# Performance work log

Hardware: AMD Instinct MI355X
Metric: run time of the kernel (lower is better)

## Reference

```python
import jax, jax.numpy as jnp
import numpy as np

NUM_ENTITIES = 100000
NUM_TIMES = 10000
D = 512
DB = 768
NUM_REL = 200
NUM_BASES = 4
N_NODES = 30000
N_EDGES = 200000
B = 128
P_ENT = 64
P_TIME = 32
T_UNIQ = 2000


def setup_inputs() -> dict:
    key = jax.random.key(0)
    ks = jax.random.split(key, 32)
    n = jax.random.normal
    ri = jax.random.randint
    inp = {}
    # learned params
    inp['emb'] = n(ks[0], (NUM_ENTITIES + NUM_TIMES, D), jnp.float32) * 0.05
    sc = 1.0 / np.sqrt(D)
    inp['basis1'] = n(ks[1], (NUM_BASES, D, D), jnp.float32) * sc
    inp['att1'] = n(ks[2], (NUM_REL, NUM_BASES), jnp.float32) * 0.5
    inp['root1'] = n(ks[3], (D, D), jnp.float32) * sc
    inp['bias1'] = jnp.zeros((D,), jnp.float32)
    inp['basis2'] = n(ks[4], (NUM_BASES, D, D), jnp.float32) * sc
    inp['att2'] = n(ks[5], (NUM_REL, NUM_BASES), jnp.float32) * 0.5
    inp['root2'] = n(ks[6], (D, D), jnp.float32) * sc
    inp['bias2'] = jnp.zeros((D,), jnp.float32)
    sb = 1.0 / np.sqrt(DB)
    inp['W_lin'] = n(ks[7], (DB, D), jnp.float32) * sb
    inp['b_lin'] = jnp.zeros((D,), jnp.float32)
    inp['W_attn'] = n(ks[8], (DB, D), jnp.float32) * sb
    inp['b_attn'] = jnp.zeros((D,), jnp.float32)
    inp['W_prob'] = n(ks[9], (DB, 1), jnp.float32) * sb
    inp['b_prob'] = jnp.zeros((1,), jnp.float32)
    # forward tensor args
    inp['ques_emb_bert'] = n(ks[10], (B, DB), jnp.float32)
    inp['x_idx'] = ri(ks[11], (N_NODES,), 0, NUM_ENTITIES, jnp.int32)
    inp['edge_index'] = ri(ks[12], (2, N_EDGES), 0, N_NODES, jnp.int32)
    inp['edge_type'] = ri(ks[13], (N_EDGES,), 0, NUM_REL, jnp.int32)
    inp['start_time'] = ri(ks[14], (N_EDGES,), 0, NUM_TIMES, jnp.int32)
    inp['end_time'] = ri(ks[15], (N_EDGES,), 0, NUM_TIMES, jnp.int32)
    inp['edge_batch_idx'] = jnp.sort(ri(ks[16], (N_EDGES,), 0, B, jnp.int32))
    inp['edge_norm'] = jax.random.uniform(ks[17], (N_EDGES,), jnp.float32)
    inp['uniq_times'] = ri(ks[18], (T_UNIQ,), 0, NUM_TIMES, jnp.int32)
    # padded index vectors: positions >= count point at the appended zero row
    ent_counts = ri(ks[19], (B,), 1, P_ENT + 1, jnp.int32)
    time_counts = ri(ks[20], (B,), 1, P_TIME + 1, jnp.int32)
    pe = ri(ks[21], (B, P_ENT), 0, N_NODES, jnp.int32)
    pt = ri(ks[22], (B, P_TIME), 0, T_UNIQ, jnp.int32)
    inp['padded_ent'] = jnp.where(jnp.arange(P_ENT)[None, :] < ent_counts[:, None], pe, N_NODES)
    inp['padded_time'] = jnp.where(jnp.arange(P_TIME)[None, :] < time_counts[:, None], pt, T_UNIQ)
    inp['ent_counts'] = ent_counts
    inp['time_counts'] = time_counts
    return inp


def rgcn_layer(x, basis, att, root, bias, src, dst, etype, st_emb, et_emb, q_t, edge_norm):
    # basis decomposition: project all nodes through each basis once. [N, NB, D]
    xb = jnp.einsum('ni,bio->nbo', x, basis)
    coeff = att[etype]                                 # [E, NB]
    msg = jnp.einsum('eb,ebd->ed', coeff, xb[src])     # [E, D]
    # time gate: question-time embedding vs edge interval midpoint embedding
    gate = jax.nn.sigmoid(jnp.sum(q_t * 0.5 * (st_emb + et_emb), axis=-1))  # [E]
    msg = msg * (gate * edge_norm)[:, None]
    agg = jax.ops.segment_sum(msg, dst, num_segments=N_NODES)
    return agg + x @ root + bias


def reference(emb, basis1, att1, root1, bias1, basis2, att2, root2, bias2,
              W_lin, b_lin, W_attn, b_attn, W_prob, b_prob,
              ques_emb_bert, x_idx, edge_index, edge_type, start_time, end_time,
              edge_batch_idx, edge_norm, uniq_times, padded_ent, padded_time,
              ent_counts, time_counts):
    question_embedding = ques_emb_bert @ W_lin + b_lin                  # [B, D]
    time_for_edge_attn = (ques_emb_bert @ W_attn + b_attn)[edge_batch_idx]  # [E, D]
    st_emb = emb[start_time + NUM_ENTITIES]
    et_emb = emb[end_time + NUM_ENTITIES]
    x = emb[x_idx]                                                      # [N, D]
    src, dst = edge_index[0], edge_index[1]
    h = jax.nn.relu(rgcn_layer(x, basis1, att1, root1, bias1, src, dst, edge_type,
                               st_emb, et_emb, time_for_edge_attn, edge_norm))
    # dropout is identity in eval mode
    h = rgcn_layer(h, basis2, att2, root2, bias2, src, dst, edge_type,
                   st_emb, et_emb, time_for_edge_attn, edge_norm)       # [N, D]
    subgraph_time_emb = emb[uniq_times + NUM_ENTITIES]                  # [T_u, D]
    zero = jnp.zeros((1, D), h.dtype)
    ent_w_zeros = jnp.concatenate([h, zero], axis=0)
    time_w_zeros = jnp.concatenate([subgraph_time_emb, zero], axis=0)
    pooled_ent = jnp.sum(ent_w_zeros[padded_ent], axis=1) / ent_counts[:, None].astype(h.dtype)
    pooled_time = jnp.sum(time_w_zeros[padded_time], axis=1) / time_counts[:, None].astype(h.dtype)
    p_ent = jax.nn.sigmoid(ques_emb_bert @ W_prob + b_prob)             # [B, 1]
    pred = (question_embedding + pooled_ent * p_ent + pooled_time * (1.0 - p_ent)) / 3.0
    # batched cosine similarity against full entity+time vocab
    pred_n = pred / jnp.maximum(jnp.linalg.norm(pred, axis=-1, keepdims=True), 1e-8)
    emb_n = emb / jnp.maximum(jnp.linalg.norm(emb, axis=-1, keepdims=True), 1e-8)
    score = pred_n @ emb_n.T                                            # [B, V]
    return score * 30.0
```

## Files before the change

### kernel.cpp

```cpp
#include <hip/hip_runtime.h>

#define NUM_ENT   100000
#define NTIMES    10000
#define DD        512
#define DB        768
#define NREL      200
#define NBAS      4
#define NN        30000
#define NEDGE     200000
#define BATCH     128
#define PENT      64
#define PTIME     32
#define TUNIQ     2000
#define V_TOT     110000
#define M_PAD2    30208
#define MT2R      1888
#define KT_L      80
#define KT_E      16
#define TCT       632

typedef __attribute__((ext_vector_type(8))) short s8v;
typedef __attribute__((ext_vector_type(4))) float f4v;

__device__ __forceinline__ unsigned short f2bf(float x){
  unsigned int u = __builtin_bit_cast(unsigned int, x);
  u += 0x7fffu + ((u >> 16) & 1u);
  return (unsigned short)(u >> 16);
}
__device__ __forceinline__ float bf2f(unsigned short h){
  unsigned int u = ((unsigned int)h) << 16;
  return __builtin_bit_cast(float, u);
}

__device__ __forceinline__ void gload16(const void* g, void* l){
  __builtin_amdgcn_global_load_lds(
      (const __attribute__((address_space(1))) void*)g,
      (__attribute__((address_space(3))) void*)l, 16, 0, 0);
}


__global__ __launch_bounds__(256) void k_small2(const float* __restrict__ ques,
    const float* __restrict__ Wl, const float* __restrict__ bl,
    const float* __restrict__ Wa, const float* __restrict__ ba,
    const float* __restrict__ Wp, const float* __restrict__ bp,
    float* __restrict__ qlin, float* __restrict__ qattn, float* __restrict__ pent){
  if (blockIdx.x == 32){
    int b = threadIdx.x >> 1, half = threadIdx.x & 1;
    float a = 0.f;
    int k0 = half * 384;
    for (int k = k0; k < k0 + 384; ++k)
      a = fmaf(ques[(size_t)b * DB + k], Wp[k], a);
    a += __shfl_xor(a, 1);
    if (half == 0) pent[b] = 1.f / (1.f + expf(-(a + bp[0])));
    return;
  }
  __shared__ float sq[128 * 96];
  int col = threadIdx.x & 31, bg = threadIdx.x >> 5;
  int c0 = blockIdx.x * 32;
  const float* W = (c0 < 512) ? Wl : Wa;
  int wcol = (c0 & 511) + col;
  float acc[16] = {};
  for (int k0 = 0; k0 < DB; k0 += 96){
    __syncthreads();
    for (int i = threadIdx.x; i < 128 * 96; i += 256){
      int b = i / 96, kk = i - b * 96;
      sq[i] = ques[(size_t)b * DB + k0 + kk];
    }
    __syncthreads();
    for (int kk = 0; kk < 96; kk += 4){
      float w0 = W[(size_t)(k0 + kk + 0) * 512 + wcol];
      float w1 = W[(size_t)(k0 + kk + 1) * 512 + wcol];
      float w2 = W[(size_t)(k0 + kk + 2) * 512 + wcol];
      float w3 = W[(size_t)(k0 + kk + 3) * 512 + wcol];
      #pragma unroll
      for (int bb = 0; bb < 16; ++bb){
        float4 qv = *reinterpret_cast<const float4*>(&sq[(bg * 16 + bb) * 96 + kk]);
        acc[bb] = fmaf(qv.x, w0, fmaf(qv.y, w1, fmaf(qv.z, w2, fmaf(qv.w, w3, acc[bb]))));
      }
    }
  }
  float* dst = (c0 < 512) ? qlin : qattn;
  const float* bias = (c0 < 512) ? bl : ba;
  #pragma unroll
  for (int bb = 0; bb < 16; ++bb)
    dst[(size_t)(bg * 16 + bb) * 512 + wcol] = acc[bb] + bias[wcol];
}

__global__ __launch_bounds__(256) void k_pack_qrows(const float* __restrict__ src,
    unsigned short* __restrict__ Ap){
  int w = (int)((blockIdx.x * 256 + threadIdx.x) >> 6);
  int lane = threadIdx.x & 63;
  if (w >= BATCH) return;
  const float* p = src + (size_t)w * 512 + lane * 8;
  s8v o;
  #pragma unroll
  for (int j = 0; j < 8; ++j) o[j] = (short)f2bf(p[j]);
  *reinterpret_cast<s8v*>(Ap + ((size_t)((w >> 4) * KT_E + (lane >> 2)) << 9)
                             + ((w & 15) + (lane & 3) * 16) * 8) = o;
}

__global__ __launch_bounds__(256) void k_pack_B(const float* __restrict__ basis,
    const float* __restrict__ root, unsigned short* __restrict__ Bp){
  int idx = blockIdx.x * 256 + threadIdx.x;
  if (idx >= KT_L * 32 * 64) return;
  int lane = idx & 63; int kt = idx >> 11;
  int k0 = kt * 32 + (lane >> 4) * 8;
  int col = ((idx >> 6) & 31) * 16 + (lane & 15);
  s8v o;
  #pragma unroll
  for (int j = 0; j < 8; ++j){
    int k = k0 + j;
    float v = (k < 2048) ? basis[(size_t)k * 512 + col] : root[(size_t)(k - 2048) * 512 + col];
    o[j] = (short)f2bf(v);
  }
  *reinterpret_cast<s8v*>(Bp + (size_t)idx * 8) = o;
}

__global__ __launch_bounds__(256) void k_pack_temb(const float* __restrict__ emb,
    unsigned short* __restrict__ Bt){
  int idx = blockIdx.x * 256 + threadIdx.x;
  if (idx >= KT_E * TCT * 64) return;
  int lane = idx & 63;
  int ct = (idx >> 6) % TCT;
  int kt = idx / (TCT * 64);
  int c = ct * 16 + (lane & 15);
  int k0 = kt * 32 + (lane >> 4) * 8;
  s8v o;
  if (c < NTIMES){
    const float* p = emb + (size_t)(NUM_ENT + c) * 512 + k0;
    #pragma unroll
    for (int j = 0; j < 8; ++j) o[j] = (short)f2bf(p[j]);
  } else {
    #pragma unroll
    for (int j = 0; j < 8; ++j) o[j] = 0;
  }
  *reinterpret_cast<s8v*>(Bt + (size_t)idx * 8) = o;
}

__global__ __launch_bounds__(256) void k_gemm_m2(
    const unsigned short* __restrict__ A, const unsigned short* __restrict__ B,
    float* __restrict__ outf){
  __shared__ __align__(1024) short sAll[3 * 8192];
  const int Kt = KT_E;
  int tid = threadIdx.x;
  int lane = tid & 63, wid = tid >> 6;
  int wr = wid >> 1, wc = wid & 1;
  int rt0 = blockIdx.x * 8;
  int ct0 = blockIdx.y * 8;
  const unsigned short* pA0 = A + ((size_t)(rt0 + 2 * wid) * Kt) * 512 + lane * 8;
  const unsigned short* pA1 = pA0 + (size_t)Kt * 512;
  const unsigned short* pB0 = B + (size_t)(ct0 + 2 * wid) * 512 + lane * 8;
  const unsigned short* pB1 = pB0 + 512;
  size_t gbs = (size_t)TCT * 512;
  int so = 2 * wid * 512;
  f4v acc[4][4] = {};

  auto STAGE = [&](int buf, int kt){
    short* b = &sAll[buf * 8192];
    gload16(pA0 + (size_t)kt * 512, b + so);
    gload16(pA1 + (size_t)kt * 512, b + so + 512);
    gload16(pB0 + (size_t)kt * gbs, b + 4096 + so);
    gload16(pB1 + (size_t)kt * gbs, b + 4096 + so + 512);
  };
  auto COMPUTE = [&](int buf){
    const short* base = &sAll[buf * 8192];
    s8v af[4], bfr[4];
    #pragma unroll
    for (int m = 0; m < 4; ++m) af[m] = *reinterpret_cast<const s8v*>(base + (wr * 4 + m) * 512 + lane * 8);
    #pragma unroll
    for (int n = 0; n < 4; ++n) bfr[n] = *reinterpret_cast<const s8v*>(base + 4096 + (wc * 4 + n) * 512 + lane * 8);
    #pragma unroll
    for (int m = 0; m < 4; ++m)
      #pragma unroll
      for (int n = 0; n < 4; ++n)
        acc[m][n] = __builtin_amdgcn_mfma_f32_16x16x32_bf16(af[m], bfr[n], acc[m][n], 0, 0, 0);
  };

  STAGE(0, 0);
  STAGE(1, 1);
  int cb = 0, sb = 2;
  for (int kt = 0; kt < Kt - 2; ++kt){
    STAGE(sb, kt + 2);
    asm volatile("s_waitcnt vmcnt(8)" ::: "memory");
    __builtin_amdgcn_s_barrier();
    __builtin_amdgcn_sched_barrier(0);
    COMPUTE(cb);
    __builtin_amdgcn_s_barrier();
    cb = (cb == 2) ? 0 : cb + 1;
    sb = (sb == 2) ? 0 : sb + 1;
  }
  asm volatile("s_waitcnt vmcnt(4)" ::: "memory");
  __builtin_amdgcn_s_barrier();
  __builtin_amdgcn_sched_barrier(0);
  COMPUTE(cb);
  cb = (cb == 2) ? 0 : cb + 1;
  asm volatile("s_waitcnt vmcnt(0)" ::: "memory");
  __builtin_amdgcn_s_barrier();
  __builtin_amdgcn_sched_barrier(0);
  COMPUTE(cb);

  #pragma unroll
  for (int m = 0; m < 4; ++m)
    #pragma unroll
    for (int n = 0; n < 4; ++n){
      int row0 = rt0 * 16 + (wr * 4 + m) * 16 + ((lane >> 4) * 4);
      int col  = (ct0 + wc * 4 + n) * 16 + (lane & 15);
      #pragma unroll
      for (int r = 0; r < 4; ++r){
        int rr = row0 + r;
        if (col < NTIMES) outf[(size_t)rr * NTIMES + col] = acc[m][n][r];
      }
    }
}

template<int MODE>
__global__ __launch_bounds__(512, 4) void k_gemm256(
    const unsigned short* __restrict__ A, const unsigned short* __restrict__ B,
    const float* __restrict__ bias, unsigned short* __restrict__ outh){
  __shared__ __align__(1024) short sAll[3 * 12288];
  const int Kt = KT_L;
  int tid = threadIdx.x;
  int lane = tid & 63, wid = tid >> 6;
  int wr = wid >> 1, wc = wid & 1;
  int g = blockIdx.x;
  int ng = (g & 7) * 59 + (g >> 3);
  int blkM = ng >> 2, blkN = ng & 3;
  int rt0 = blkM * 16;
  int ct0 = blkN * 8;
  const unsigned short* pA0 = A + ((size_t)(rt0 + wid) * Kt) * 512 + lane * 8;
  const unsigned short* pA1 = A + ((size_t)(rt0 + 8 + wid) * Kt) * 512 + lane * 8;
  const unsigned short* pB0 = B + (size_t)(ct0 + wid) * 512 + lane * 8;
  const size_t gbs = 32 * 512;
  int soA0 = wid * 512, soA1 = (8 + wid) * 512, soB = 8192 + wid * 512;
  f4v acc[4][4] = {};

  auto STAGE = [&](int buf, int kt){
    short* b = &sAll[buf * 12288];
    gload16(pA0 + (size_t)kt * 512, b + soA0);
    gload16(pA1 + (size_t)kt * 512, b + soA1);
    gload16(pB0 + (size_t)kt * gbs, b + soB);
  };
  auto COMPUTE = [&](int buf){
    const short* base = &sAll[buf * 12288];
    s8v af[4], bfr[4];
    #pragma unroll
    for (int m = 0; m < 4; ++m) af[m] = *reinterpret_cast<const s8v*>(base + (wr * 4 + m) * 512 + lane * 8);
    #pragma unroll
    for (int n = 0; n < 4; ++n) bfr[n] = *reinterpret_cast<const s8v*>(base + 8192 + (wc * 4 + n) * 512 + lane * 8);
    __builtin_amdgcn_s_setprio(1);
    #pragma unroll
    for (int m = 0; m < 4; ++m)
      #pragma unroll
      for (int n = 0; n < 4; ++n)
        acc[m][n] = __builtin_amdgcn_mfma_f32_16x16x32_bf16(af[m], bfr[n], acc[m][n], 0, 0, 0);
    __builtin_amdgcn_s_setprio(0);
  };

  STAGE(0, 0);
  STAGE(1, 1);
  int cb = 0, sb = 2;
  for (int kt = 0; kt < Kt - 2; ++kt){
    STAGE(sb, kt + 2);
    asm volatile("s_waitcnt vmcnt(6)" ::: "memory");
    __builtin_amdgcn_s_barrier();
    __builtin_amdgcn_sched_barrier(0);
    COMPUTE(cb);
    __builtin_amdgcn_s_barrier();
    cb = (cb == 2) ? 0 : cb + 1;
    sb = (sb == 2) ? 0 : sb + 1;
  }
  asm volatile("s_waitcnt vmcnt(3)" ::: "memory");
  __builtin_amdgcn_s_barrier();
  __builtin_amdgcn_sched_barrier(0);
  COMPUTE(cb);
  cb = (cb == 2) ? 0 : cb + 1;
  asm volatile("s_waitcnt vmcnt(0)" ::: "memory");
  __builtin_amdgcn_s_barrier();
  __builtin_amdgcn_sched_barrier(0);
  COMPUTE(cb);

  int R0 = blkM * 256 + wr * 64 + (lane >> 4) * 4;
  int C0 = blkN * 128 + wc * 64 + (lane & 15);
  #pragma unroll
  for (int m = 0; m < 4; ++m)
    #pragma unroll
    for (int r4 = 0; r4 < 4; ++r4){
      int rr = R0 + m * 16 + r4;
      if (rr < NN){
        #pragma unroll
        for (int n = 0; n < 4; ++n){
          int col = C0 + n * 16;
          float v = acc[m][n][r4] + bias[col];
          if constexpr (MODE == 1) v = fmaxf(v, 0.f);
          outh[(size_t)rr * 512 + col] = f2bf(v);
        }
// ... 77 lines not shown
    s8v xv = *reinterpret_cast<const s8v*>(xsrc + (size_t)s0 * 512 + lane * 8);
    for (int j = 0; j < deg; ++j){
      s8v xn = xv;
      if (j + 1 < deg){
        int sn = __shfl(my_s, j + 1);
        xn = *reinterpret_cast<const s8v*>(xsrc + (size_t)sn * 512 + lane * 8);
      }
      float c0 = __shfl(c0l, j), c1 = __shfl(c1l, j);
      float c2 = __shfl(c2l, j), c3 = __shfl(c3l, j);
      #pragma unroll
      for (int jj = 0; jj < 8; ++jj){
        float x = bf2f((unsigned short)xv[jj]);
        acc[0][jj] = fmaf(c0, x, acc[0][jj]);
        acc[1][jj] = fmaf(c1, x, acc[1][jj]);
        acc[2][jj] = fmaf(c2, x, acc[2][jj]);
        acc[3][jj] = fmaf(c3, x, acc[3][jj]);
      }
      xv = xn;
    }
  }
  #pragma unroll
  for (int b = 0; b < NBAS; ++b){
    s8v o;
    #pragma unroll
    for (int jj = 0; jj < 8; ++jj) o[jj] = (short)f2bf(acc[b][jj]);
    *reinterpret_cast<s8v*>(Ap + ((size_t)(n >> 4) * KT_L + b * 16 + (lane >> 2)) * 512
                               + ((n & 15) + (lane & 3) * 16) * 8) = o;
  }
}

__global__ __launch_bounds__(256) void k_pred(const unsigned short* __restrict__ h2,
    const float* __restrict__ emb, const int* __restrict__ uniq,
    const int* __restrict__ pent_idx, const int* __restrict__ ptime_idx,
    const int* __restrict__ ent_c, const int* __restrict__ time_c,
    const float* __restrict__ qlin, const float* __restrict__ pent,
    unsigned short* __restrict__ Ap_pred){
  __shared__ float sacc[4][512];
  int b = blockIdx.x;
  int wid = threadIdx.x >> 6, lane = threadIdx.x & 63;
  float a[8] = {};
  if (wid < 2){
    for (int j = wid * 32; j < wid * 32 + 32; ++j){
      int idx = pent_idx[b * PENT + j];
      if (idx < NN){
        s8v hv = *reinterpret_cast<const s8v*>(h2 + (size_t)idx * 512 + lane * 8);
        #pragma unroll
        for (int jj = 0; jj < 8; ++jj) a[jj] += bf2f((unsigned short)hv[jj]);
      }
    }
  } else {
    for (int j = (wid - 2) * 16; j < (wid - 2) * 16 + 16; ++j){
      int ti = ptime_idx[b * PTIME + j];
      if (ti < TUNIQ){
        const float* p = emb + (size_t)(NUM_ENT + uniq[ti]) * 512 + lane * 8;
        #pragma unroll
        for (int jj = 0; jj < 8; ++jj) a[jj] += p[jj];
      }
    }
  }
  #pragma unroll
  for (int jj = 0; jj < 8; ++jj) sacc[wid][lane * 8 + jj] = a[jj];
  __syncthreads();
  if (wid == 0){
    float ce = 1.f / (float)ent_c[b], ct = 1.f / (float)time_c[b];
    float p = pent[b];
    float pr[8]; float ss = 0.f;
    #pragma unroll
    for (int jj = 0; jj < 8; ++jj){
      int i = lane * 8 + jj;
      float ae = sacc[0][i] + sacc[1][i];
      float at = sacc[2][i] + sacc[3][i];
      float v = (qlin[(size_t)b * 512 + i] + ae * ce * p + at * ct * (1.f - p)) * (1.f / 3.f);
      pr[jj] = v; ss += v * v;
    }
    ss += __shfl_xor(ss, 32); ss += __shfl_xor(ss, 16); ss += __shfl_xor(ss, 8);
    ss += __shfl_xor(ss, 4);  ss += __shfl_xor(ss, 2);  ss += __shfl_xor(ss, 1);
    float inv = 1.f / fmaxf(sqrtf(ss), 1e-8f);
    s8v o;
    #pragma unroll
    for (int jj = 0; jj < 8; ++jj) o[jj] = (short)f2bf(pr[jj] * inv);
    *reinterpret_cast<s8v*>(Ap_pred + ((size_t)((b >> 4) * KT_E + (lane >> 2)) << 9)
                                    + ((b & 15) + (lane & 3) * 16) * 8) = o;
  }
}

__global__ __launch_bounds__(256, 3) void k_score(
    const unsigned short* __restrict__ Apred, const float* __restrict__ emb,
    float* __restrict__ out){
  __shared__ __align__(1024) short sB[2][4096];
  __shared__ float sf[256];
  int tid = threadIdx.x;
  int lane = tid & 63, wid = tid >> 6;
  int wr = wid >> 1, wc = wid & 1;
  int c0 = blockIdx.x * 128;
  int bc = tid & 127;
  int kh = tid >> 7;
  int colg = c0 + bc;
  bool cval = colg < V_TOT;
  const float* gB = emb + (size_t)colg * 512 + kh * 16;
  int wb0 = (bc >> 4) * 512 + ((2 * kh) * 16 + (bc & 15)) * 8;
  int wb1 = wb0 + 128;
  float ss = 0.f;
  float4 q0, q1, q2, q3;
  f4v acc[4][4] = {};

  auto LOADB = [&](int s){
    if (cval){
      const float4* p = reinterpret_cast<const float4*>(gB + (size_t)s * 32);
      q0 = p[0]; q1 = p[1]; q2 = p[2]; q3 = p[3];
    } else {
      q0 = q1 = q2 = q3 = float4{0.f, 0.f, 0.f, 0.f};
    }
  };
  auto WRITEB = [&](int p){
    short* bb = &sB[p][0];
    s8v o0, o1;
    o0[0] = (short)f2bf(q0.x); o0[1] = (short)f2bf(q0.y); o0[2] = (short)f2bf(q0.z); o0[3] = (short)f2bf(q0.w);
    o0[4] = (short)f2bf(q1.x); o0[5] = (short)f2bf(q1.y); o0[6] = (short)f2bf(q1.z); o0[7] = (short)f2bf(q1.w);
    o1[0] = (short)f2bf(q2.x); o1[1] = (short)f2bf(q2.y); o1[2] = (short)f2bf(q2.z); o1[3] = (short)f2bf(q2.w);
    o1[4] = (short)f2bf(q3.x); o1[5] = (short)f2bf(q3.y); o1[6] = (short)f2bf(q3.z); o1[7] = (short)f2bf(q3.w);
    ss += q0.x*q0.x + q0.y*q0.y + q0.z*q0.z + q0.w*q0.w;
    ss += q1.x*q1.x + q1.y*q1.y + q1.z*q1.z + q1.w*q1.w;
    ss += q2.x*q2.x + q2.y*q2.y + q2.z*q2.z + q2.w*q2.w;
    ss += q3.x*q3.x + q3.y*q3.y + q3.z*q3.z + q3.w*q3.w;
    *reinterpret_cast<s8v*>(bb + wb0) = o0;
    *reinterpret_cast<s8v*>(bb + wb1) = o1;
  };
  auto COMPUTE = [&](int p, int s){
    s8v af[4], bfr[4];
    #pragma unroll
    for (int m = 0; m < 4; ++m)
      af[m] = *reinterpret_cast<const s8v*>(
          Apred + (((size_t)(wr * 4 + m) * KT_E + s) << 9) + lane * 8);
    #pragma unroll
    for (int n = 0; n < 4; ++n)
      bfr[n] = *reinterpret_cast<const s8v*>(&sB[p][(wc * 4 + n) * 512 + lane * 8]);
    #pragma unroll
    for (int m = 0; m < 4; ++m)
      #pragma unroll
      for (int n = 0; n < 4; ++n)
        acc[m][n] = __builtin_amdgcn_mfma_f32_16x16x32_bf16(af[m], bfr[n], acc[m][n], 0, 0, 0);
  };

  LOADB(0);
  for (int s = 0; s < 16; ++s){
    int p = s & 1;
    WRITEB(p);
    __syncthreads();
    if (s < 15) LOADB(s + 1);
    COMPUTE(p, s);
    __syncthreads();
  }
  sf[tid] = ss;
  __syncthreads();

  int R0 = wr * 64 + (lane >> 4) * 4;
  int C0l = wc * 64 + (lane & 15);
  float inv[4];
  #pragma unroll
  for (int n = 0; n < 4; ++n){
    int cl = C0l + n * 16;
    float s2 = sf[cl] + sf[cl + 128];
    inv[n] = (1.f / fmaxf(sqrtf(s2), 1e-8f)) * 30.0f;
  }
  bool cok = (c0 + 127) < V_TOT;
  #pragma unroll
  for (int m = 0; m < 4; ++m)
    #pragma unroll
    for (int r4 = 0; r4 < 4; ++r4){
      int rr = R0 + m * 16 + r4;
      float* orow = out + (size_t)rr * V_TOT + c0 + C0l;
      if (cok){
        #pragma unroll
        for (int n = 0; n < 4; ++n) orow[n * 16] = acc[m][n][r4] * inv[n];
      } else {
        #pragma unroll
        for (int n = 0; n < 4; ++n)
          if (c0 + C0l + n * 16 < V_TOT) orow[n * 16] = acc[m][n][r4] * inv[n];
      }
    }
}

extern "C" void kernel_launch(void* const* d_in, const int* in_sizes, int n_in,
                              void* d_out, int out_size, void* d_ws, size_t ws_size,
                              hipStream_t stream){
  const float* emb    = (const float*)d_in[0];
  const float* basis1 = (const float*)d_in[1];
  const float* att1   = (const float*)d_in[2];
  const float* root1  = (const float*)d_in[3];
  const float* bias1  = (const float*)d_in[4];
  const float* basis2 = (const float*)d_in[5];
  const float* att2   = (const float*)d_in[6];
  const float* root2  = (const float*)d_in[7];
  const float* bias2  = (const float*)d_in[8];
  const float* W_lin  = (const float*)d_in[9];
  const float* b_lin  = (const float*)d_in[10];
  const float* W_attn = (const float*)d_in[11];
  const float* b_attn = (const float*)d_in[12];
  const float* W_prob = (const float*)d_in[13];
  const float* b_prob = (const float*)d_in[14];
  const float* ques   = (const float*)d_in[15];
  const int* x_idx    = (const int*)d_in[16];
  const int* eidx     = (const int*)d_in[17];
  const int* etype    = (const int*)d_in[18];
  const int* stime    = (const int*)d_in[19];
  const int* etime    = (const int*)d_in[20];
  const int* ebatch   = (const int*)d_in[21];
  const float* enorm  = (const float*)d_in[22];
  const int* uniq     = (const int*)d_in[23];
  const int* pent_i   = (const int*)d_in[24];
  const int* ptime_i  = (const int*)d_in[25];
  const int* ent_c    = (const int*)d_in[26];
  const int* time_c   = (const int*)d_in[27];
  float* out = (float*)d_out;

  char* w = (char*)d_ws;
  size_t off = 0;
  auto alloc = [&](size_t bytes)->char*{ char* p = w + off; off += (bytes + 255) & ~(size_t)255; return p; };
  unsigned short* Ap   = (unsigned short*)alloc((size_t)MT2R * KT_L * 1024);
  unsigned short* B1p  = (unsigned short*)alloc((size_t)KT_L * 32 * 1024);
  unsigned short* B2p  = (unsigned short*)alloc((size_t)KT_L * 32 * 1024);
  unsigned short* Bt   = (unsigned short*)alloc((size_t)KT_E * TCT * 1024);
  char* xh_base = alloc((size_t)NN * 512 * 2 * 2);
  unsigned short* x_rm = (unsigned short*)xh_base;
  unsigned short* h1   = (unsigned short*)(xh_base + (size_t)NN * 512 * 2);
  unsigned short* h2   = (unsigned short*)xh_base;
  float* M2    = (float*)alloc((size_t)BATCH * NTIMES * 4);
  float* we    = (float*)alloc((size_t)NEDGE * 4);
  float* qlin  = (float*)alloc((size_t)BATCH * 512 * 4);
  float* qattn = (float*)alloc((size_t)BATCH * 512 * 4);
  float* pent  = (float*)alloc(1024);
  unsigned short* Apq    = (unsigned short*)alloc((size_t)8 * KT_E * 1024);
  unsigned short* Appred = (unsigned short*)alloc((size_t)8 * KT_E * 1024);
  int* cnt   = (int*)alloc((size_t)NN * 4);
  int* lists = (int*)alloc((size_t)NN * 64 * 4);
  (void)ws_size; (void)in_sizes; (void)n_in; (void)out_size;

  k_small2<<<33, 256, 0, stream>>>(ques, W_lin, b_lin, W_attn, b_attn, W_prob, b_prob,
                                   qlin, qattn, pent);
  k_pack_qrows<<<32, 256, 0, stream>>>(qattn, Apq);
  k_pack_B<<<(KT_L * 32 * 64 + 255) / 256, 256, 0, stream>>>(basis1, root1, B1p);
  k_pack_B<<<(KT_L * 32 * 64 + 255) / 256, 256, 0, stream>>>(basis2, root2, B2p);
  k_pack_temb<<<(KT_E * TCT * 64) / 256, 256, 0, stream>>>(emb, Bt);
  k_gemm_m2<<<dim3(1, 79), 256, 0, stream>>>(Apq, Bt, M2);
  hipMemsetAsync(cnt, 0, (size_t)NN * 4, stream);
  k_edgeprep<<<(NEDGE + 255) / 256, 256, 0, stream>>>(ebatch, stime, etime, enorm, M2,
                                                      eidx, we, cnt, lists);
  k_gather_x<<<NN / 4, 256, 0, stream>>>(x_idx, emb, Ap, x_rm);
  k_edge_agg<<<NN / 4, 256, 0, stream>>>(x_rm, eidx, etype, we, att1, cnt, lists, Ap);
  k_gemm256<1><<<472, 512, 0, stream>>>(Ap, B1p, bias1, h1);
  k_pack_rows<<<NN / 4, 256, 0, stream>>>(h1, Ap);
  k_edge_agg<<<NN / 4, 256, 0, stream>>>(h1, eidx, etype, we, att2, cnt, lists, Ap);
  k_gemm256<2><<<472, 512, 0, stream>>>(Ap, B2p, bias2, h2);
  k_pred<<<BATCH, 256, 0, stream>>>(h2, emb, uniq, pent_i, ptime_i, ent_c, time_c,
                                    qlin, pent, Appred);
  k_score<<<860, 256, 0, stream>>>(Appred, emb, out);
}
```

Baseline: 713.3 us.

## Replace packed time-embedding GEMM and score GEMM with LDS-free column-per-wave GEMM

Adds a templated k_colgemm in which each wavefront owns 32 vocabulary columns. It streams fp32 embedding rows straight from global memory into registers, converts them to bf16 and feeds MFMA, while the A fragments (128 query rows) are read directly from global memory. This one kernel replaces both the time-embedding pack plus M2 GEMM and the final cosine-score kernel, which removes a pack pass, a workspace buffer and LDS staging and barriers. In exchange, A fragments are re-read from global/L2 by every wave, and the store pattern writes scattered 4-byte values per row.

```diff
diff --git a/kernel.cpp b/kernel.cpp
--- a/kernel.cpp
+++ b/kernel.cpp
@@ -17,7 +17,6 @@
 #define MT2R      1888
 #define KT_L      80
 #define KT_E      16
-#define TCT       632
 
 typedef __attribute__((ext_vector_type(8))) short s8v;
 typedef __attribute__((ext_vector_type(4))) float f4v;
@@ -116,100 +115,86 @@
   *reinterpret_cast<s8v*>(Bp + (size_t)idx * 8) = o;
 }
 
-__global__ __launch_bounds__(256) void k_pack_temb(const float* __restrict__ emb,
-    unsigned short* __restrict__ Bt){
-  int idx = blockIdx.x * 256 + threadIdx.x;
-  if (idx >= KT_E * TCT * 64) return;
-  int lane = idx & 63;
-  int ct = (idx >> 6) % TCT;
-  int kt = idx / (TCT * 64);
-  int c = ct * 16 + (lane & 15);
-  int k0 = kt * 32 + (lane >> 4) * 8;
-  s8v o;
-  if (c < NTIMES){
-    const float* p = emb + (size_t)(NUM_ENT + c) * 512 + k0;
-    #pragma unroll
-    for (int j = 0; j < 8; ++j) o[j] = (short)f2bf(p[j]);
-  } else {
-    #pragma unroll
-    for (int j = 0; j < 8; ++j) o[j] = 0;
-  }
-  *reinterpret_cast<s8v*>(Bt + (size_t)idx * 8) = o;
-}
-
-__global__ __launch_bounds__(256) void k_gemm_m2(
-    const unsigned short* __restrict__ A, const unsigned short* __restrict__ B,
-    float* __restrict__ outf){
-  __shared__ __align__(1024) short sAll[3 * 8192];
-  const int Kt = KT_E;
-  int tid = threadIdx.x;
-  int lane = tid & 63, wid = tid >> 6;
-  int wr = wid >> 1, wc = wid & 1;
-  int rt0 = blockIdx.x * 8;
-  int ct0 = blockIdx.y * 8;
-  const unsigned short* pA0 = A + ((size_t)(rt0 + 2 * wid) * Kt) * 512 + lane * 8;
-  const unsigned short* pA1 = pA0 + (size_t)Kt * 512;
-  const unsigned short* pB0 = B + (size_t)(ct0 + 2 * wid) * 512 + lane * 8;
-  const unsigned short* pB1 = pB0 + 512;
-  size_t gbs = (size_t)TCT * 512;
-  int so = 2 * wid * 512;
-  f4v acc[4][4] = {};
-
-  auto STAGE = [&](int buf, int kt){
-    short* b = &sAll[buf * 8192];
-    gload16(pA0 + (size_t)kt * 512, b + so);
-    gload16(pA1 + (size_t)kt * 512, b + so + 512);
-    gload16(pB0 + (size_t)kt * gbs, b + 4096 + so);
-    gload16(pB1 + (size_t)kt * gbs, b + 4096 + so + 512);
-  };
-  auto COMPUTE = [&](int buf){
-    const short* base = &sAll[buf * 8192];
-    s8v af[4], bfr[4];
-    #pragma unroll
-    for (int m = 0; m < 4; ++m) af[m] = *reinterpret_cast<const s8v*>(base + (wr * 4 + m) * 512 + lane * 8);
-    #pragma unroll
-    for (int n = 0; n < 4; ++n) bfr[n] = *reinterpret_cast<const s8v*>(base + 4096 + (wc * 4 + n) * 512 + lane * 8);
-    #pragma unroll
-    for (int m = 0; m < 4; ++m)
-      #pragma unroll
-      for (int n = 0; n < 4; ++n)
-        acc[m][n] = __builtin_amdgcn_mfma_f32_16x16x32_bf16(af[m], bfr[n], acc[m][n], 0, 0, 0);
-  };
-
-  STAGE(0, 0);
-  STAGE(1, 1);
-  int cb = 0, sb = 2;
-  for (int kt = 0; kt < Kt - 2; ++kt){
-    STAGE(sb, kt + 2);
-    asm volatile("s_waitcnt vmcnt(8)" ::: "memory");
-    __builtin_amdgcn_s_barrier();
-    __builtin_amdgcn_sched_barrier(0);
-    COMPUTE(cb);
-    __builtin_amdgcn_s_barrier();
-    cb = (cb == 2) ? 0 : cb + 1;
-    sb = (sb == 2) ? 0 : sb + 1;
-  }
-  asm volatile("s_waitcnt vmcnt(4)" ::: "memory");
-  __builtin_amdgcn_s_barrier();
-  __builtin_amdgcn_sched_barrier(0);
-  COMPUTE(cb);
-  cb = (cb == 2) ? 0 : cb + 1;
-  asm volatile("s_waitcnt vmcnt(0)" ::: "memory");
-  __builtin_amdgcn_s_barrier();
-  __builtin_amdgcn_sched_barrier(0);
-  COMPUTE(cb);
-
-  #pragma unroll
-  for (int m = 0; m < 4; ++m)
-    #pragma unroll
-    for (int n = 0; n < 4; ++n){
-      int row0 = rt0 * 16 + (wr * 4 + m) * 16 + ((lane >> 4) * 4);
-      int col  = (ct0 + wc * 4 + n) * 16 + (lane & 15);
-      #pragma unroll
-      for (int r = 0; r < 4; ++r){
-        int rr = row0 + r;
-        if (col < NTIMES) outf[(size_t)rr * NTIMES + col] = acc[m][n][r];
-      }
+template<int NORM>
+__global__ __launch_bounds__(256, 4) void k_colgemm(
+    const unsigned short* __restrict__ Ap, const float* __restrict__ embbase,
+    float* __restrict__ out, int ncols, int ldout){
+  int lane = threadIdx.x & 63, wid = threadIdx.x >> 6;
+  int w32 = (blockIdx.x * 4 + wid) * 32;
+  if (w32 >= ncols) return;
+  int r16 = lane & 15, kq = lane >> 4;
+  int c0 = w32 + r16, c1 = w32 + 16 + r16;
+  bool rv0 = c0 < ncols, rv1 = c1 < ncols;
+  const float* gB0 = embbase + (size_t)c0 * 512 + kq * 8;
+  const float* gB1 = embbase + (size_t)c1 * 512 + kq * 8;
+  f4v acc0[8], acc1[8];
+  #pragma unroll
+  for (int m = 0; m < 8; ++m){ acc0[m] = f4v{0,0,0,0}; acc1[m] = f4v{0,0,0,0}; }
+  float ss0 = 0.f, ss1 = 0.f;
+  float cu0[8], cu1[8], nx0[8], nx1[8];
+
+  #pragma unroll
+  for (int j = 0; j < 4; ++j){
+    float4 a0 = rv0 ? reinterpret_cast<const float4*>(gB0)[j & 1 ? 1 : 0]
+                    : float4{0,0,0,0};
+    (void)a0;
+  }
+  {
+    float4 a0 = rv0 ? reinterpret_cast<const float4*>(gB0)[0] : float4{0,0,0,0};
+    float4 a1 = rv0 ? reinterpret_cast<const float4*>(gB0)[1] : float4{0,0,0,0};
+    float4 b0 = rv1 ? reinterpret_cast<const float4*>(gB1)[0] : float4{0,0,0,0};
+    float4 b1 = rv1 ? reinterpret_cast<const float4*>(gB1)[1] : float4{0,0,0,0};
+    cu0[0]=a0.x; cu0[1]=a0.y; cu0[2]=a0.z; cu0[3]=a0.w;
+    cu0[4]=a1.x; cu0[5]=a1.y; cu0[6]=a1.z; cu0[7]=a1.w;
+    cu1[0]=b0.x; cu1[1]=b0.y; cu1[2]=b0.z; cu1[3]=b0.w;
+    cu1[4]=b1.x; cu1[5]=b1.y; cu1[6]=b1.z; cu1[7]=b1.w;
+  }
+  #pragma unroll
+  for (int kt = 0; kt < 16; ++kt){
+    if (kt < 15){
+      const float4* p0 = reinterpret_cast<const float4*>(gB0 + (kt + 1) * 32);
+      const float4* p1 = reinterpret_cast<const float4*>(gB1 + (kt + 1) * 32);
+      float4 a0 = rv0 ? p0[0] : float4{0,0,0,0};
+      float4 a1 = rv0 ? p0[1] : float4{0,0,0,0};
+      float4 b0 = rv1 ? p1[0] : float4{0,0,0,0};
+      float4 b1 = rv1 ? p1[1] : float4{0,0,0,0};
+      nx0[0]=a0.x; nx0[1]=a0.y; nx0[2]=a0.z; nx0[3]=a0.w;
+      nx0[4]=a1.x; nx0[5]=a1.y; nx0[6]=a1.z; nx0[7]=a1.w;
+      nx1[0]=b0.x; nx1[1]=b0.y; nx1[2]=b0.z; nx1[3]=b0.w;
+      nx1[4]=b1.x; nx1[5]=b1.y; nx1[6]=b1.z; nx1[7]=b1.w;
+    }
+    s8v bf0, bf1;
+    #pragma unroll
+    for (int j = 0; j < 8; ++j){
+      ss0 = fmaf(cu0[j], cu0[j], ss0);
+      ss1 = fmaf(cu1[j], cu1[j], ss1);
+      bf0[j] = (short)f2bf(cu0[j]);
+      bf1[j] = (short)f2bf(cu1[j]);
+    }
+    #pragma unroll
+    for (int m = 0; m < 8; ++m){
+      s8v af = *reinterpret_cast<const s8v*>(Ap + ((size_t)(m * KT_E + kt) << 9) + lane * 8);
+      acc0[m] = __builtin_amdgcn_mfma_f32_16x16x32_bf16(af, bf0, acc0[m], 0, 0, 0);
+      acc1[m] = __builtin_amdgcn_mfma_f32_16x16x32_bf16(af, bf1, acc1[m], 0, 0, 0);
+    }
+    #pragma unroll
+    for (int j = 0; j < 8; ++j){ cu0[j] = nx0[j]; cu1[j] = nx1[j]; }
+  }
+  float inv0 = 1.f, inv1 = 1.f;
+  if constexpr (NORM){
+    ss0 += __shfl_xor(ss0, 16); ss0 += __shfl_xor(ss0, 32);
+    ss1 += __shfl_xor(ss1, 16); ss1 += __shfl_xor(ss1, 32);
+    inv0 = 30.f / fmaxf(sqrtf(ss0), 1e-8f);
+    inv1 = 30.f / fmaxf(sqrtf(ss1), 1e-8f);
+  }
+  #pragma unroll
+  for (int m = 0; m < 8; ++m)
+    #pragma unroll
+    for (int r = 0; r < 4; ++r){
+      int row = m * 16 + kq * 4 + r;
+      float* orow = out + (size_t)row * ldout;
+      if (rv0) orow[c0] = acc0[m][r] * inv0;
+      if (rv1) orow[c1] = acc1[m][r] * inv1;
     }
 }
 
@@ -456,103 +441,6 @@
   }
 }
 
-__global__ __launch_bounds__(256, 3) void k_score(
-    const unsigned short* __restrict__ Apred, const float* __restrict__ emb,
-    float* __restrict__ out){
-  __shared__ __align__(1024) short sB[2][4096];
-  __shared__ float sf[256];
-  int tid = threadIdx.x;
-  int lane = tid & 63, wid = tid >> 6;
-  int wr = wid >> 1, wc = wid & 1;
-  int c0 = blockIdx.x * 128;
-  int bc = tid & 127;
-  int kh = tid >> 7;
-  int colg = c0 + bc;
-  bool cval = colg < V_TOT;
-  const float* gB = emb + (size_t)colg * 512 + kh * 16;
-  int wb0 = (bc >> 4) * 512 + ((2 * kh) * 16 + (bc & 15)) * 8;
-  int wb1 = wb0 + 128;
-  float ss = 0.f;
-  float4 q0, q1, q2, q3;
-  f4v acc[4][4] = {};
-
-  auto LOADB = [&](int s){
-    if (cval){
-      const float4* p = reinterpret_cast<const float4*>(gB + (size_t)s * 32);
-      q0 = p[0]; q1 = p[1]; q2 = p[2]; q3 = p[3];
-    } else {
-      q0 = q1 = q2 = q3 = float4{0.f, 0.f, 0.f, 0.f};
-    }
-  };
-  auto WRITEB = [&](int p){
-    short* bb = &sB[p][0];
-    s8v o0, o1;
-    o0[0] = (short)f2bf(q0.x); o0[1] = (short)f2bf(q0.y); o0[2] = (short)f2bf(q0.z); o0[3] = (short)f2bf(q0.w);
-    o0[4] = (short)f2bf(q1.x); o0[5] = (short)f2bf(q1.y); o0[6] = (short)f2bf(q1.z); o0[7] = (short)f2bf(q1.w);
-    o1[0] = (short)f2bf(q2.x); o1[1] = (short)f2bf(q2.y); o1[2] = (short)f2bf(q2.z); o1[3] = (short)f2bf(q2.w);
-    o1[4] = (short)f2bf(q3.x); o1[5] = (short)f2bf(q3.y); o1[6] = (short)f2bf(q3.z); o1[7] = (short)f2bf(q3.w);
-    ss += q0.x*q0.x + q0.y*q0.y + q0.z*q0.z + q0.w*q0.w;
-    ss += q1.x*q1.x + q1.y*q1.y + q1.z*q1.z + q1.w*q1.w;
-    ss += q2.x*q2.x + q2.y*q2.y + q2.z*q2.z + q2.w*q2.w;
-    ss += q3.x*q3.x + q3.y*q3.y + q3.z*q3.z + q3.w*q3.w;
-    *reinterpret_cast<s8v*>(bb + wb0) = o0;
-    *reinterpret_cast<s8v*>(bb + wb1) = o1;
-  };
-  auto COMPUTE = [&](int p, int s){
-    s8v af[4], bfr[4];
-    #pragma unroll
-    for (int m = 0; m < 4; ++m)
-      af[m] = *reinterpret_cast<const s8v*>(
-          Apred + (((size_t)(wr * 4 + m) * KT_E + s) << 9) + lane * 8);
-    #pragma unroll
-    for (int n = 0; n < 4; ++n)
-      bfr[n] = *reinterpret_cast<const s8v*>(&sB[p][(wc * 4 + n) * 512 + lane * 8]);
-    #pragma unroll
-    for (int m = 0; m < 4; ++m)
-      #pragma unroll
-      for (int n = 0; n < 4; ++n)
-        acc[m][n] = __builtin_amdgcn_mfma_f32_16x16x32_bf16(af[m], bfr[n], acc[m][n], 0, 0, 0);
-  };
-
-  LOADB(0);
-  for (int s = 0; s < 16; ++s){
-    int p = s & 1;
-    WRITEB(p);
-    __syncthreads();
-    if (s < 15) LOADB(s + 1);
-    COMPUTE(p, s);
-    __syncthreads();
-  }
-  sf[tid] = ss;
-  __syncthreads();
-
-  int R0 = wr * 64 + (lane >> 4) * 4;
-  int C0l = wc * 64 + (lane & 15);
-  float inv[4];
-  #pragma unroll
-  for (int n = 0; n < 4; ++n){
-    int cl = C0l + n * 16;
-    float s2 = sf[cl] + sf[cl + 128];
-    inv[n] = (1.f / fmaxf(sqrtf(s2), 1e-8f)) * 30.0f;
-  }
-  bool cok = (c0 + 127) < V_TOT;
-  #pragma unroll
-  for (int m = 0; m < 4; ++m)
-    #pragma unroll
-    for (int r4 = 0; r4 < 4; ++r4){
-      int rr = R0 + m * 16 + r4;
-      float* orow = out + (size_t)rr * V_TOT + c0 + C0l;
-      if (cok){
-        #pragma unroll
-        for (int n = 0; n < 4; ++n) orow[n * 16] = acc[m][n][r4] * inv[n];
-      } else {
-        #pragma unroll
-        for (int n = 0; n < 4; ++n)
-          if (c0 + C0l + n * 16 < V_TOT) orow[n * 16] = acc[m][n][r4] * inv[n];
-      }
-    }
-}
-
 extern "C" void kernel_launch(void* const* d_in, const int* in_sizes, int n_in,
                               void* d_out, int out_size, void* d_ws, size_t ws_size,
                               hipStream_t stream){
@@ -592,7 +480,6 @@
   unsigned short* Ap   = (unsigned short*)alloc((size_t)MT2R * KT_L * 1024);
   unsigned short* B1p  = (unsigned short*)alloc((size_t)KT_L * 32 * 1024);
   unsigned short* B2p  = (unsigned short*)alloc((size_t)KT_L * 32 * 1024);
-  unsigned short* Bt   = (unsigned short*)alloc((size_t)KT_E * TCT * 1024);
   char* xh_base = alloc((size_t)NN * 512 * 2 * 2);
   unsigned short* x_rm = (unsigned short*)xh_base;
   unsigned short* h1   = (unsigned short*)(xh_base + (size_t)NN * 512 * 2);
@@ -613,8 +500,8 @@
   k_pack_qrows<<<32, 256, 0, stream>>>(qattn, Apq);
   k_pack_B<<<(KT_L * 32 * 64 + 255) / 256, 256, 0, stream>>>(basis1, root1, B1p);
   k_pack_B<<<(KT_L * 32 * 64 + 255) / 256, 256, 0, stream>>>(basis2, root2, B2p);
-  k_pack_temb<<<(KT_E * TCT * 64) / 256, 256, 0, stream>>>(emb, Bt);
-  k_gemm_m2<<<dim3(1, 79), 256, 0, stream>>>(Apq, Bt, M2);
+  k_colgemm<0><<<(10000 / 32 + 4) / 4, 256, 0, stream>>>(
+      Apq, emb + (size_t)NUM_ENT * 512, M2, NTIMES, NTIMES);
   hipMemsetAsync(cnt, 0, (size_t)NN * 4, stream);
   k_edgeprep<<<(NEDGE + 255) / 256, 256, 0, stream>>>(ebatch, stime, etime, enorm, M2,
                                                       eidx, we, cnt, lists);
@@ -626,5 +513,6 @@
   k_gemm256<2><<<472, 512, 0, stream>>>(Ap, B2p, bias2, h2);
   k_pred<<<BATCH, 256, 0, stream>>>(h2, emb, uniq, pent_i, ptime_i, ent_c, time_c,
                                     qlin, pent, Appred);
-  k_score<<<860, 256, 0, stream>>>(Appred, emb, out);
-}
+  k_colgemm<1><<<(V_TOT / 32 + 4) / 4, 256, 0, stream>>>(
+      Appred, emb, out, V_TOT, V_TOT);
+}
```

New measurement: 895.3 us. +25.5%, slower.

## Pre-pack full embedding table to bf16 tiles and share with time GEMM and scoring

Applied to the files above, without the earlier changes.

Adds a conversion kernel that converts the full entity+time embedding table to bf16 in MFMA tile layout once and computes per-row inverse norms. The time-embedding GEMM now reads its slice of that packed table, which removes the separate time-embedding pack. The final scoring kernel is replaced by a pipelined async global-to-LDS GEMM that stages both operands through LDS and writes coalesced float4 output through an LDS transpose. This costs an extra round trip of the bf16 table through memory (about 110MB written and read back) in exchange for a simpler, better pipelined scoring loop.

```diff
diff --git a/kernel.cpp b/kernel.cpp
--- a/kernel.cpp
+++ b/kernel.cpp
@@ -13,11 +13,12 @@
 #define PTIME     32
 #define TUNIQ     2000
 #define V_TOT     110000
+#define V_PAD     110208
+#define VT16      6888
 #define M_PAD2    30208
 #define MT2R      1888
 #define KT_L      80
 #define KT_E      16
-#define TCT       632
 
 typedef __attribute__((ext_vector_type(8))) short s8v;
 typedef __attribute__((ext_vector_type(4))) float f4v;
@@ -38,6 +39,43 @@
       (__attribute__((address_space(3))) void*)l, 16, 0, 0);
 }
 
+
+__global__ __launch_bounds__(256) void k_conv_emb(const float* __restrict__ emb,
+    unsigned short* __restrict__ Bp, float* __restrict__ invn){
+  int vt = blockIdx.x;
+  int wid = threadIdx.x >> 6, lane = threadIdx.x & 63;
+  int vrow = vt * 16 + (lane & 15);
+  float ss = 0.f;
+  __shared__ float ssw[4][16];
+  for (int i = 0; i < 4; ++i){
+    int kt = wid + i * 4;
+    int k0 = kt * 32 + (lane >> 4) * 8;
+    s8v o;
+    if (vrow < V_TOT){
+      const float4* p = reinterpret_cast<const float4*>(emb + (size_t)vrow * DD + k0);
+      float4 v0 = p[0], v1 = p[1];
+      ss += v0.x*v0.x + v0.y*v0.y + v0.z*v0.z + v0.w*v0.w;
+      ss += v1.x*v1.x + v1.y*v1.y + v1.z*v1.z + v1.w*v1.w;
+      o[0] = (short)f2bf(v0.x); o[1] = (short)f2bf(v0.y);
+      o[2] = (short)f2bf(v0.z); o[3] = (short)f2bf(v0.w);
+      o[4] = (short)f2bf(v1.x); o[5] = (short)f2bf(v1.y);
+      o[6] = (short)f2bf(v1.z); o[7] = (short)f2bf(v1.w);
+    } else {
+      #pragma unroll
+      for (int j = 0; j < 8; ++j) o[j] = 0;
+    }
+    *reinterpret_cast<s8v*>(Bp + ((size_t)(kt * VT16 + vt) << 9) + lane * 8) = o;
+  }
+  ss += __shfl_xor(ss, 16);
+  ss += __shfl_xor(ss, 32);
+  if ((lane >> 4) == 0) ssw[wid][lane] = ss;
+  __syncthreads();
+  if (threadIdx.x < 16){
+    float s = ssw[0][threadIdx.x] + ssw[1][threadIdx.x] + ssw[2][threadIdx.x] + ssw[3][threadIdx.x];
+    int v = vt * 16 + threadIdx.x;
+    invn[v] = (v < V_TOT) ? (1.0f / fmaxf(sqrtf(s), 1e-8f)) : 0.0f;
+  }
+}
 
 __global__ __launch_bounds__(256) void k_small2(const float* __restrict__ ques,
     const float* __restrict__ Wl, const float* __restrict__ bl,
@@ -116,27 +154,6 @@
   *reinterpret_cast<s8v*>(Bp + (size_t)idx * 8) = o;
 }
 
-__global__ __launch_bounds__(256) void k_pack_temb(const float* __restrict__ emb,
-    unsigned short* __restrict__ Bt){
-  int idx = blockIdx.x * 256 + threadIdx.x;
-  if (idx >= KT_E * TCT * 64) return;
-  int lane = idx & 63;
-  int ct = (idx >> 6) % TCT;
-  int kt = idx / (TCT * 64);
-  int c = ct * 16 + (lane & 15);
-  int k0 = kt * 32 + (lane >> 4) * 8;
-  s8v o;
-  if (c < NTIMES){
-    const float* p = emb + (size_t)(NUM_ENT + c) * 512 + k0;
-    #pragma unroll
-    for (int j = 0; j < 8; ++j) o[j] = (short)f2bf(p[j]);
-  } else {
-    #pragma unroll
-    for (int j = 0; j < 8; ++j) o[j] = 0;
-  }
-  *reinterpret_cast<s8v*>(Bt + (size_t)idx * 8) = o;
-}
-
 __global__ __launch_bounds__(256) void k_gemm_m2(
     const unsigned short* __restrict__ A, const unsigned short* __restrict__ B,
     float* __restrict__ outf){
@@ -151,7 +168,7 @@
   const unsigned short* pA1 = pA0 + (size_t)Kt * 512;
   const unsigned short* pB0 = B + (size_t)(ct0 + 2 * wid) * 512 + lane * 8;
   const unsigned short* pB1 = pB0 + 512;
-  size_t gbs = (size_t)TCT * 512;
+  size_t gbs = (size_t)VT16 * 512;
   int so = 2 * wid * 512;
   f4v acc[4][4] = {};
 
@@ -211,6 +228,102 @@
         if (col < NTIMES) outf[(size_t)rr * NTIMES + col] = acc[m][n][r];
       }
     }
+}
+
+__global__ __launch_bounds__(256, 3) void k_score_p(
+    const unsigned short* __restrict__ Apred, const unsigned short* __restrict__ Bp,
+    const float* __restrict__ invn, float* __restrict__ out){
+  __shared__ __align__(1024) short sAll[3 * 8192];
+  const int Kt = KT_E;
+  int tid = threadIdx.x;
+  int lane = tid & 63, wid = tid >> 6;
+  int wr = wid >> 1, wc = wid & 1;
+  int kq = lane >> 4, r16 = lane & 15;
+  int ct0 = blockIdx.x * 8;
+  const unsigned short* pA0 = Apred + ((size_t)(2 * wid) * Kt) * 512 + lane * 8;
+  const unsigned short* pA1 = pA0 + (size_t)Kt * 512;
+  const unsigned short* pB0 = Bp + (size_t)(ct0 + 2 * wid) * 512 + lane * 8;
+  const unsigned short* pB1 = pB0 + 512;
+  size_t gbs = (size_t)VT16 * 512;
+  int so = 2 * wid * 512;
+  f4v acc[4][4] = {};
+
+  auto STAGE = [&](int buf, int kt){
+    short* b = &sAll[buf * 8192];
+    gload16(pA0 + (size_t)kt * 512, b + so);
+    gload16(pA1 + (size_t)kt * 512, b + so + 512);
+    gload16(pB0 + (size_t)kt * gbs, b + 4096 + so);
+    gload16(pB1 + (size_t)kt * gbs, b + 4096 + so + 512);
+  };
+  auto COMPUTE = [&](int buf){
+    const short* base = &sAll[buf * 8192];
+    s8v af[4], bfr[4];
+    #pragma unroll
+    for (int m = 0; m < 4; ++m) af[m] = *reinterpret_cast<const s8v*>(base + (wr * 4 + m) * 512 + lane * 8);
+    #pragma unroll
+    for (int n = 0; n < 4; ++n) bfr[n] = *reinterpret_cast<const s8v*>(base + 4096 + (wc * 4 + n) * 512 + lane * 8);
+    #pragma unroll
+    for (int m = 0; m < 4; ++m)
+      #pragma unroll
+      for (int n = 0; n < 4; ++n)
+        acc[m][n] = __builtin_amdgcn_mfma_f32_16x16x32_bf16(af[m], bfr[n], acc[m][n], 0, 0, 0);
+  };
+
+  STAGE(0, 0);
+  STAGE(1, 1);
+  int cb = 0, sb = 2;
+  for (int kt = 0; kt < Kt - 2; ++kt){
+    STAGE(sb, kt + 2);
+    asm volatile("s_waitcnt vmcnt(8)" ::: "memory");
+    __builtin_amdgcn_s_barrier();
+    __builtin_amdgcn_sched_barrier(0);
+    COMPUTE(cb);
+    __builtin_amdgcn_s_barrier();
+    cb = (cb == 2) ? 0 : cb + 1;
+    sb = (sb == 2) ? 0 : sb + 1;
+  }
+  asm volatile("s_waitcnt vmcnt(4)" ::: "memory");
+  __builtin_amdgcn_s_barrier();
+  __builtin_amdgcn_sched_barrier(0);
+  COMPUTE(cb);
+  cb = (cb == 2) ? 0 : cb + 1;
+  asm volatile("s_waitcnt vmcnt(0)" ::: "memory");
+  __builtin_amdgcn_s_barrier();
+  __builtin_amdgcn_sched_barrier(0);
+  COMPUTE(cb);
+
+  __syncthreads();
+  float* scratch = reinterpret_cast<float*>(sAll) + wid * 2176;
+  int colg = ct0 * 16 + wc * 64 + r16 * 4;
+  bool c_ok = colg < V_TOT;
+  float4 inv4 = float4{0.f, 0.f, 0.f, 0.f};
+  if (c_ok){
+    inv4 = *reinterpret_cast<const float4*>(invn + colg);
+    inv4.x *= 30.f; inv4.y *= 30.f; inv4.z *= 30.f; inv4.w *= 30.f;
+  }
+  #pragma unroll
+  for (int p = 0; p < 2; ++p){
+    #pragma unroll
+    for (int mm = 0; mm < 2; ++mm){
+      int m = p * 2 + mm;
+      #pragma unroll
+      for (int n = 0; n < 4; ++n)
+        #pragma unroll
+        for (int r = 0; r < 4; ++r)
+          scratch[(mm * 16 + kq * 4 + r) * 68 + n * 16 + r16] = acc[m][n][r];
+    }
+    #pragma unroll
+    for (int i = 0; i < 8; ++i){
+      int row_r = i * 4 + kq;
+      float4 v = *reinterpret_cast<const float4*>(scratch + row_r * 68 + r16 * 4);
+      if (c_ok){
+        float4 o;
+        o.x = v.x * inv4.x; o.y = v.y * inv4.y; o.z = v.z * inv4.z; o.w = v.w * inv4.w;
+        int grr = wr * 64 + p * 32 + row_r;
+        *reinterpret_cast<float4*>(out + (size_t)grr * V_TOT + colg) = o;
+      }
+    }
+  }
 }
 
 template<int MODE>
@@ -454,103 +567,6 @@
     *reinterpret_cast<s8v*>(Ap_pred + ((size_t)((b >> 4) * KT_E + (lane >> 2)) << 9)
                                     + ((b & 15) + (lane & 3) * 16) * 8) = o;
   }
-}
-
-__global__ __launch_bounds__(256, 3) void k_score(
-    const unsigned short* __restrict__ Apred, const float* __restrict__ emb,
-    float* __restrict__ out){
-  __shared__ __align__(1024) short sB[2][4096];
-  __shared__ float sf[256];
-  int tid = threadIdx.x;
-  int lane = tid & 63, wid = tid >> 6;
-  int wr = wid >> 1, wc = wid & 1;
-  int c0 = blockIdx.x * 128;
-  int bc = tid & 127;
-  int kh = tid >> 7;
-  int colg = c0 + bc;
-  bool cval = colg < V_TOT;
-  const float* gB = emb + (size_t)colg * 512 + kh * 16;
-  int wb0 = (bc >> 4) * 512 + ((2 * kh) * 16 + (bc & 15)) * 8;
-  int wb1 = wb0 + 128;
-  float ss = 0.f;
-  float4 q0, q1, q2, q3;
-  f4v acc[4][4] = {};
-
-  auto LOADB = [&](int s){
-    if (cval){
-      const float4* p = reinterpret_cast<const float4*>(gB + (size_t)s * 32);
-      q0 = p[0]; q1 = p[1]; q2 = p[2]; q3 = p[3];
-    } else {
-      q0 = q1 = q2 = q3 = float4{0.f, 0.f, 0.f, 0.f};
-    }
-  };
-  auto WRITEB = [&](int p){
-    short* bb = &sB[p][0];
-    s8v o0, o1;
-    o0[0] = (short)f2bf(q0.x); o0[1] = (short)f2bf(q0.y); o0[2] = (short)f2bf(q0.z); o0[3] = (short)f2bf(q0.w);
-    o0[4] = (short)f2bf(q1.x); o0[5] = (short)f2bf(q1.y); o0[6] = (short)f2bf(q1.z); o0[7] = (short)f2bf(q1.w);
-    o1[0] = (short)f2bf(q2.x); o1[1] = (short)f2bf(q2.y); o1[2] = (short)f2bf(q2.z); o1[3] = (short)f2bf(q2.w);
-    o1[4] = (short)f2bf(q3.x); o1[5] = (short)f2bf(q3.y); o1[6] = (short)f2bf(q3.z); o1[7] = (short)f2bf(q3.w);
-    ss += q0.x*q0.x + q0.y*q0.y + q0.z*q0.z + q0.w*q0.w;
-    ss += q1.x*q1.x + q1.y*q1.y + q1.z*q1.z + q1.w*q1.w;
-    ss += q2.x*q2.x + q2.y*q2.y + q2.z*q2.z + q2.w*q2.w;
-    ss += q3.x*q3.x + q3.y*q3.y + q3.z*q3.z + q3.w*q3.w;
-    *reinterpret_cast<s8v*>(bb + wb0) = o0;
-    *reinterpret_cast<s8v*>(bb + wb1) = o1;
-  };
-  auto COMPUTE = [&](int p, int s){
-    s8v af[4], bfr[4];
-    #pragma unroll
-    for (int m = 0; m < 4; ++m)
-      af[m] = *reinterpret_cast<const s8v*>(
-          Apred + (((size_t)(wr * 4 + m) * KT_E + s) << 9) + lane * 8);
-    #pragma unroll
-    for (int n = 0; n < 4; ++n)
-      bfr[n] = *reinterpret_cast<const s8v*>(&sB[p][(wc * 4 + n) * 512 + lane * 8]);
-    #pragma unroll
-    for (int m = 0; m < 4; ++m)
-      #pragma unroll
-      for (int n = 0; n < 4; ++n)
-        acc[m][n] = __builtin_amdgcn_mfma_f32_16x16x32_bf16(af[m], bfr[n], acc[m][n], 0, 0, 0);
-  };
-
-  LOADB(0);
-  for (int s = 0; s < 16; ++s){
-    int p = s & 1;
-    WRITEB(p);
-    __syncthreads();
-    if (s < 15) LOADB(s + 1);
-    COMPUTE(p, s);
-    __syncthreads();
-  }
-  sf[tid] = ss;
-  __syncthreads();
-
-  int R0 = wr * 64 + (lane >> 4) * 4;
-  int C0l = wc * 64 + (lane & 15);
-  float inv[4];
-  #pragma unroll
-  for (int n = 0; n < 4; ++n){
-    int cl = C0l + n * 16;
-    float s2 = sf[cl] + sf[cl + 128];
-    inv[n] = (1.f / fmaxf(sqrtf(s2), 1e-8f)) * 30.0f;
-  }
-  bool cok = (c0 + 127) < V_TOT;
-  #pragma unroll
-  for (int m = 0; m < 4; ++m)
-    #pragma unroll
-    for (int r4 = 0; r4 < 4; ++r4){
-      int rr = R0 + m * 16 + r4;
-      float* orow = out + (size_t)rr * V_TOT + c0 + C0l;
-      if (cok){
-        #pragma unroll
-        for (int n = 0; n < 4; ++n) orow[n * 16] = acc[m][n][r4] * inv[n];
-      } else {
-        #pragma unroll
-        for (int n = 0; n < 4; ++n)
-          if (c0 + C0l + n * 16 < V_TOT) orow[n * 16] = acc[m][n][r4] * inv[n];
-      }
-    }
 }
 
 extern "C" void kernel_launch(void* const* d_in, const int* in_sizes, int n_in,
@@ -589,10 +605,11 @@
   char* w = (char*)d_ws;
   size_t off = 0;
   auto alloc = [&](size_t bytes)->char*{ char* p = w + off; off += (bytes + 255) & ~(size_t)255; return p; };
+  unsigned short* Bp_emb = (unsigned short*)alloc((size_t)KT_E * VT16 * 1024);
+  float*          invn   = (float*)alloc((size_t)V_PAD * 4);
   unsigned short* Ap   = (unsigned short*)alloc((size_t)MT2R * KT_L * 1024);
   unsigned short* B1p  = (unsigned short*)alloc((size_t)KT_L * 32 * 1024);
   unsigned short* B2p  = (unsigned short*)alloc((size_t)KT_L * 32 * 1024);
-  unsigned short* Bt   = (unsigned short*)alloc((size_t)KT_E * TCT * 1024);
   char* xh_base = alloc((size_t)NN * 512 * 2 * 2);
   unsigned short* x_rm = (unsigned short*)xh_base;
   unsigned short* h1   = (unsigned short*)(xh_base + (size_t)NN * 512 * 2);
@@ -611,10 +628,10 @@
   k_small2<<<33, 256, 0, stream>>>(ques, W_lin, b_lin, W_attn, b_attn, W_prob, b_prob,
                                    qlin, qattn, pent);
   k_pack_qrows<<<32, 256, 0, stream>>>(qattn, Apq);
+  k_conv_emb<<<VT16, 256, 0, stream>>>(emb, Bp_emb, invn);
   k_pack_B<<<(KT_L * 32 * 64 + 255) / 256, 256, 0, stream>>>(basis1, root1, B1p);
   k_pack_B<<<(KT_L * 32 * 64 + 255) / 256, 256, 0, stream>>>(basis2, root2, B2p);
-  k_pack_temb<<<(KT_E * TCT * 64) / 256, 256, 0, stream>>>(emb, Bt);
-  k_gemm_m2<<<dim3(1, 79), 256, 0, stream>>>(Apq, Bt, M2);
+  k_gemm_m2<<<dim3(1, 79), 256, 0, stream>>>(Apq, Bp_emb + (size_t)6250 * 512, M2);
   hipMemsetAsync(cnt, 0, (size_t)NN * 4, stream);
   k_edgeprep<<<(NEDGE + 255) / 256, 256, 0, stream>>>(ebatch, stime, etime, enorm, M2,
                                                       eidx, we, cnt, lists);
@@ -626,5 +643,5 @@
   k_gemm256<2><<<472, 512, 0, stream>>>(Ap, B2p, bias2, h2);
   k_pred<<<BATCH, 256, 0, stream>>>(h2, emb, uniq, pent_i, ptime_i, ent_c, time_c,
                                     qlin, pent, Appred);
-  k_score<<<860, 256, 0, stream>>>(Appred, emb, out);
-}
+  k_score_p<<<861, 256, 0, stream>>>(Appred, Bp_emb, invn, out);
+}
```

After: 685.6 us. -3.9%, faster.
